# Optimization experiments

Measured on AMD Instinct MI355X. Metric: run time of the kernel, lower is better.

## Reference

```python
import jax, jax.numpy as jnp
import numpy as np

D_MODEL = 1024
N_HEADS = 16
D_FF = 4096
HEAD_DIM = D_MODEL // N_HEADS
LN_EPS = 1e-5


def layer_norm(x, g, b):
    m = jnp.mean(x, axis=-1, keepdims=True)
    v = jnp.mean(jnp.square(x - m), axis=-1, keepdims=True)
    return (x - m) * jax.lax.rsqrt(v + LN_EPS) * g + b


def setup_inputs() -> dict:
    key = jax.random.key(0)
    ks = jax.random.split(key, 16)
    s = 0.02
    d = {
        'x': jax.random.normal(ks[0], (4, 2048, D_MODEL), jnp.float32),
        'Wq': jax.random.normal(ks[1], (D_MODEL, D_MODEL), jnp.float32) * s,
        'bq': jnp.zeros((D_MODEL,), jnp.float32),
        'Wk': jax.random.normal(ks[2], (D_MODEL, D_MODEL), jnp.float32) * s,
        'bk': jnp.zeros((D_MODEL,), jnp.float32),
        'Wv': jax.random.normal(ks[3], (D_MODEL, D_MODEL), jnp.float32) * s,
        'bv': jnp.zeros((D_MODEL,), jnp.float32),
        'Wo': jax.random.normal(ks[4], (D_MODEL, D_MODEL), jnp.float32) * s,
        'bo': jnp.zeros((D_MODEL,), jnp.float32),
        'W1': jax.random.normal(ks[5], (D_FF, D_MODEL), jnp.float32) * s,
        'b1': jnp.zeros((D_FF,), jnp.float32),
        'W2': jax.random.normal(ks[6], (D_MODEL, D_FF), jnp.float32) * s,
        'b2': jnp.zeros((D_MODEL,), jnp.float32),
        'g1': jnp.ones((D_MODEL,), jnp.float32),
        'be1': jnp.zeros((D_MODEL,), jnp.float32),
        'g2': jnp.ones((D_MODEL,), jnp.float32),
        'be2': jnp.zeros((D_MODEL,), jnp.float32),
    }
    return d


def reference(x, Wq, bq, Wk, bk, Wv, bv, Wo, bo, W1, b1, W2, b2, g1, be1, g2, be2):
    B, S, D = x.shape
    H, hd = N_HEADS, HEAD_DIM
    # QKV projections; chunk along d_model -> heads (same as reshape last dim)
    q = (x @ Wq.T + bq).reshape(B, S, H, hd)
    k = (x @ Wk.T + bk).reshape(B, S, H, hd)
    v = (x @ Wv.T + bv).reshape(B, S, H, hd)
    # scaled dot-product attention (no mask, dropout = identity in eval)
    scores = jnp.einsum('bqhd,bkhd->bhqk', q, k) / jnp.sqrt(jnp.float32(hd))
    attn = jax.nn.softmax(scores, axis=-1)
    ctx = jnp.einsum('bhqk,bkhd->bqhd', attn, v).reshape(B, S, D)
    out1 = ctx @ Wo.T + bo
    out = layer_norm(x + out1, g1, be1)
    out2 = jax.nn.relu(out @ W1.T + b1) @ W2.T + b2
    # NOTE: faithful to source bug: second residual uses out1, not out
    return layer_norm(out1 + out2, g2, be2)
```

## Files before the change

kernel.cpp:

```cpp
#include <hip/hip_runtime.h>

typedef __bf16 bf16_t;
typedef __bf16 bf16x8 __attribute__((ext_vector_type(8)));
typedef __bf16 bf16x4 __attribute__((ext_vector_type(4)));
typedef float  f32x4  __attribute__((ext_vector_type(4)));

#define SEQ   2048
#define DMODEL 1024
#define DFF   4096
#define NHEAD 16
#define HDIM  64
#define MTOK  8192

#define QSCALE 0.18033688f
#define THR_LOG2 11.5f

#define MB (size_t)(1024*1024)
static const size_t XB_OFF   = 0;
static const size_t Q_OFF    = 16*MB;
static const size_t K_OFF    = 32*MB;
static const size_t VT_OFF   = 48*MB;
static const size_t FFN1_OFF = 0;
static const size_t CTX_OFF  = 64*MB;
static const size_t OUT1_OFF = 80*MB;
static const size_t LN1_OFF  = 112*MB;
static const size_t WQKV_OFF = 128*MB;
static const size_t WO_OFF   = 134*MB;
static const size_t W1_OFF   = 136*MB;
static const size_t W2_OFF   = 144*MB;

__device__ inline void gload16(const void* g, void* l) {
    __builtin_amdgcn_global_load_lds((__attribute__((address_space(1))) void*)g,
                                     (__attribute__((address_space(3))) void*)l, 16, 0, 0);
}

__global__ __launch_bounds__(256) void cast_bf16_k(const float* __restrict__ s,
                                                   bf16_t* __restrict__ d, int n8) {
    int i = blockIdx.x * 256 + threadIdx.x;
    if (i >= n8) return;
    float4 v0 = ((const float4*)s)[2*i];
    float4 v1 = ((const float4*)s)[2*i+1];
    bf16x8 o;
    o[0]=(bf16_t)v0.x; o[1]=(bf16_t)v0.y; o[2]=(bf16_t)v0.z; o[3]=(bf16_t)v0.w;
    o[4]=(bf16_t)v1.x; o[5]=(bf16_t)v1.y; o[6]=(bf16_t)v1.z; o[7]=(bf16_t)v1.w;
    *(bf16x8*)(d + (size_t)i*8) = o;
}

__global__ __launch_bounds__(256) void concat_bias_k(const float* __restrict__ a,
                                                     const float* __restrict__ b,
                                                     const float* __restrict__ c,
                                                     float* __restrict__ o) {
    int i = blockIdx.x * 256 + threadIdx.x;
    o[i] = (i < 1024) ? a[i] : ((i < 2048) ? b[i - 1024] : c[i - 2048]);
}

template<int EPI>
__global__ __launch_bounds__(256, 2) void gemm_bt(
    const bf16_t* __restrict__ A, const bf16_t* __restrict__ Bm,
    const float* __restrict__ bias, void* __restrict__ out,
    const float* __restrict__ aux, int M, int N, int K, float scale)
{
    __shared__ bf16_t As[128*64];
    __shared__ bf16_t Bs[128*64];
    const int tid = threadIdx.x;
    const int l   = tid & 63;
    const int wid = tid >> 6;
    const int wm  = wid >> 1, wn = wid & 1;
    const int c16 = l & 15,   g  = l >> 4;
    int lin = blockIdx.y * gridDim.x + blockIdx.x;
    int nwg = gridDim.x * gridDim.y;
    int swz = (lin & 7) * (nwg >> 3) + (lin >> 3);
    const long brow = (long)(swz / gridDim.x) * 128;
    const long bcol = (long)(swz % gridDim.x) * 128;

    f32x4 acc[4][4] = {};

    const int nkt = K >> 6;
    for (int kt = 0; kt < nkt; ++kt) {
        __syncthreads();
        const bf16_t* Ag = A  + brow * K + kt*64;
        const bf16_t* Bg = Bm + bcol * K + kt*64;
#pragma unroll
        for (int c = 0; c < 4; ++c) {
            int e   = (c*256 + tid) * 8;
            int row = e >> 6;
            int col = e & 63;
            gload16(Ag + (long)row*K + col, &As[e]);
            gload16(Bg + (long)row*K + col, &Bs[e]);
        }
        __syncthreads();
#pragma unroll
        for (int kk = 0; kk < 2; ++kk) {
            bf16x8 af[4], bfr[4];
#pragma unroll
            for (int mi = 0; mi < 4; ++mi)
                af[mi] = *(const bf16x8*)&As[(wm*64 + mi*16 + c16)*64 + kk*32 + 8*g];
#pragma unroll
            for (int ni = 0; ni < 4; ++ni)
                bfr[ni] = *(const bf16x8*)&Bs[(wn*64 + ni*16 + c16)*64 + kk*32 + 8*g];
#pragma unroll
            for (int mi = 0; mi < 4; ++mi)
#pragma unroll
                for (int ni = 0; ni < 4; ++ni)
                    acc[mi][ni] = __builtin_amdgcn_mfma_f32_16x16x32_bf16(
                        af[mi], bfr[ni], acc[mi][ni], 0, 0, 0);
        }
    }

#pragma unroll
    for (int ni = 0; ni < 4; ++ni) {
        const long c = bcol + wn*64 + ni*16 + c16;
        const float bv = bias[c];
#pragma unroll
        for (int mi = 0; mi < 4; ++mi) {
#pragma unroll
            for (int i = 0; i < 4; ++i) {
                const long r = brow + wm*64 + mi*16 + g*4 + i;
                float v = (acc[mi][ni][i] + bv) * scale;
                if constexpr (EPI == 2) {
                    ((float*)out)[r*N + c] = v;
                } else {
                    ((float*)out)[r*N + c] = v + aux[r*N + c];
                }
            }
        }
    }
}

template<int EPI>
__global__ __launch_bounds__(512, 2) void gemm256(
    const bf16_t* __restrict__ A, const bf16_t* __restrict__ Bm,
    const float* __restrict__ bias, void* __restrict__ out,
    void* __restrict__ out_k, void* __restrict__ out_v,
    int M, int N, int K)
{
    __shared__ alignas(16) char lds[131072];
    const int tid = threadIdx.x;
    const int l   = tid & 63;
    const int wid = tid >> 6;
    const int wm  = wid >> 2, wn = wid & 3;
    const int c16 = l & 15,   g  = l >> 4;
    const int xsw = (c16 & 7) << 4;

    int lin = blockIdx.y * gridDim.x + blockIdx.x;
    int nwg = gridDim.x * gridDim.y;
    int swz = (lin & 7) * (nwg >> 3) + (lin >> 3);
    const long brow = (long)(swz / gridDim.x) * 256;
    const long bcol = (long)(swz % gridDim.x) * 256;

    const int rowloc = tid >> 3;
    const int srcblk = (tid & 7) ^ ((tid >> 3) & 7);
    const bf16_t* Asrc = A  + (brow + rowloc) * (long)K + srcblk * 8;
    const bf16_t* Bsrc = Bm + (bcol + rowloc) * (long)K + srcblk * 8;

    f32x4 acc[8][4] = {};
    const int NKT = K >> 6;

    auto stA = [&](int cur, int t, int j) {
        gload16(Asrc + (long)j*64*K + (long)t*64, lds + cur*65536 + j*8192 + tid*16);
    };
    auto stB = [&](int cur, int t, int j) {
        gload16(Bsrc + (long)j*64*K + (long)t*64, lds + cur*65536 + 32768 + j*8192 + tid*16);
    };

#pragma unroll
    for (int j = 0; j < 4; ++j) stA(0, 0, j);
#pragma unroll
    for (int j = 0; j < 4; ++j) stB(0, 0, j);
#pragma unroll
    for (int j = 0; j < 4; ++j) stA(1, 1, j);
#pragma unroll
    for (int j = 0; j < 4; ++j) stB(1, 1, j);
    asm volatile("s_waitcnt vmcnt(8)" ::: "memory");
    __builtin_amdgcn_sched_barrier(0);
    __builtin_amdgcn_s_barrier();

    int cur = 0;
    for (int t = 0; t < NKT; ++t, cur ^= 1) {
        const char* aL = lds + cur*65536;
        const char* bL = aL + 32768;
        const bool stg = (t + 2 < NKT);
        bf16x8 a0[4][2], a1[4][2], b0[2][2], b1[2][2];

#pragma unroll
        for (int mi = 0; mi < 4; ++mi)
#pragma unroll
            for (int kk = 0; kk < 2; ++kk)
                a0[mi][kk] = *(const bf16x8*)(aL + (wm*128 + mi*16 + c16)*128 + ((kk*64 + 16*g) ^ xsw));
#pragma unroll
        for (int ni = 0; ni < 2; ++ni)
#pragma unroll
            for (int kk = 0; kk < 2; ++kk)
                b0[ni][kk] = *(const bf16x8*)(bL + (wn*64 + ni*16 + c16)*128 + ((kk*64 + 16*g) ^ xsw));
        __builtin_amdgcn_s_barrier();
        asm volatile("s_waitcnt lgkmcnt(0)" ::: "memory");
        __builtin_amdgcn_sched_barrier(0);
        __builtin_amdgcn_s_setprio(1);
#pragma unroll
        for (int mi = 0; mi < 4; ++mi)
#pragma unroll
            for (int ni = 0; ni < 2; ++ni)
#pragma unroll
                for (int kk = 0; kk < 2; ++kk)
                    acc[mi][ni] = __builtin_amdgcn_mfma_f32_16x16x32_bf16(a0[mi][kk], b0[ni][kk], acc[mi][ni], 0, 0, 0);
        __builtin_amdgcn_s_setprio(0);
        __builtin_amdgcn_s_barrier();

#pragma unroll
        for (int ni = 0; ni < 2; ++ni)
#pragma unroll
            for (int kk = 0; kk < 2; ++kk)
                b1[ni][kk] = *(const bf16x8*)(bL + (wn*64 + (ni+2)*16 + c16)*128 + ((kk*64 + 16*g) ^ xsw));
        if (stg) { stA(cur, t+2, 0); stA(cur, t+2, 2); }
        __builtin_amdgcn_s_barrier();
        asm volatile("s_waitcnt lgkmcnt(0)" ::: "memory");
        __builtin_amdgcn_sched_barrier(0);
        __builtin_amdgcn_s_setprio(1);
#pragma unroll
        for (int mi = 0; mi < 4; ++mi)
#pragma unroll
            for (int ni = 0; ni < 2; ++ni)
#pragma unroll
                for (int kk = 0; kk < 2; ++kk)
                    acc[mi][ni+2] = __builtin_amdgcn_mfma_f32_16x16x32_bf16(a0[mi][kk], b1[ni][kk], acc[mi][ni+2], 0, 0, 0);
        __builtin_amdgcn_s_setprio(0);
        __builtin_amdgcn_s_barrier();

#pragma unroll
        for (int mi = 0; mi < 4; ++mi)
#pragma unroll
            for (int kk = 0; kk < 2; ++kk)
                a1[mi][kk] = *(const bf16x8*)(aL + (wm*128 + (mi+4)*16 + c16)*128 + ((kk*64 + 16*g) ^ xsw));
        if (stg) { stB(cur, t+2, 0); stB(cur, t+2, 1); }
        __builtin_amdgcn_s_barrier();
        asm volatile("s_waitcnt lgkmcnt(0)" ::: "memory");
        __builtin_amdgcn_sched_barrier(0);
        __builtin_amdgcn_s_setprio(1);
#pragma unroll
        for (int mi = 0; mi < 4; ++mi)
#pragma unroll
            for (int ni = 0; ni < 2; ++ni)
#pragma unroll
                for (int kk = 0; kk < 2; ++kk)
                    acc[mi+4][ni] = __builtin_amdgcn_mfma_f32_16x16x32_bf16(a1[mi][kk], b0[ni][kk], acc[mi+4][ni], 0, 0, 0);
        __builtin_amdgcn_s_setprio(0);
        __builtin_amdgcn_s_barrier();

        if (stg) { stA(cur, t+2, 1); stA(cur, t+2, 3); stB(cur, t+2, 2); stB(cur, t+2, 3); }
        __builtin_amdgcn_s_barrier();
        __builtin_amdgcn_s_setprio(1);
#pragma unroll
        for (int mi = 0; mi < 4; ++mi)
#pragma unroll
            for (int ni = 0; ni < 2; ++ni)
#pragma unroll
                for (int kk = 0; kk < 2; ++kk)
                    acc[mi+4][ni+2] = __builtin_amdgcn_mfma_f32_16x16x32_bf16(a1[mi][kk], b1[ni][kk], acc[mi+4][ni+2], 0, 0, 0);
        __builtin_amdgcn_s_setprio(0);
        if (stg)                asm volatile("s_waitcnt vmcnt(8)" ::: "memory");
        else if (t < NKT - 1)   asm volatile("s_waitcnt vmcnt(0)" ::: "memory");
        __builtin_amdgcn_sched_barrier(0);
        __builtin_amdgcn_s_barrier();
    }

#pragma unroll
    for (int ni = 0; ni < 4; ++ni) {
        const long c = bcol + wn*64 + ni*16 + c16;
        const float bv = bias[c];
#pragma unroll
        for (int mi = 0; mi < 8; ++mi) {
#pragma unroll
            for (int i = 0; i < 4; ++i) {
                const long r = brow + wm*128 + mi*16 + g*4 + i;
                float v = acc[mi][ni][i] + bv;
                if constexpr (EPI == 3) {
                    ((bf16_t*)out)[r*N + c] = (bf16_t)fmaxf(v, 0.f);
                } else {
                    const int mat = (int)(c >> 10);
                    const int hc  = (int)(c & 1023);
                    const long bb = r >> 11, sidx = r & (SEQ-1);
                    const long hb = bb*NHEAD + (hc >> 6);
                    if (mat == 0)
                        ((bf16_t*)out)[(hb*SEQ + sidx)*HDIM + (hc & 63)] = (bf16_t)(v * QSCALE);
                    else if (mat == 1)
                        ((bf16_t*)out_k)[(hb*SEQ + sidx)*HDIM + (hc & 63)] = (bf16_t)v;
                    else
                        ((bf16_t*)out_v)[(hb*HDIM + (hc & 63))*SEQ + sidx] = (bf16_t)v;
                }
            }
        }
    }
}

__device__ __forceinline__ void kload(bf16x8 (&dst)[4][2], const bf16_t* kb0,
                                      int ktt, int c16, int g) {
    const bf16_t* kbase = kb0 + (size_t)ktt*64*HDIM;
#pragma unroll
    for (int jk = 0; jk < 4; ++jk)
#pragma unroll
        for (int ks = 0; ks < 2; ++ks)
            dst[jk][ks] = *(const bf16x8*)(kbase + (size_t)(16*jk + c16)*HDIM + ks*32 + 8*g);
}

__device__ __forceinline__ void vload(bf16x8 (&vr)[4][2], const bf16_t* vt0,
                                      int ktt, int c16, int g) {
#pragma unroll
    for (int nf = 0; nf < 4; ++nf)
#pragma unroll
        for (int ks = 0; ks < 2; ++ks)
            vr[nf][ks] = *(const bf16x8*)(vt0 + (size_t)(16*nf + c16)*SEQ + ktt*64 + ks*32 + 8*g);
}

__device__ __forceinline__ void qk1(f32x4 (&s)[4], const bf16x8 (&kr)[4][2],
                                    const bf16x8 (&aqf)[2]) {
    const f32x4 z = {0.f, 0.f, 0.f, 0.f};
    __builtin_amdgcn_s_setprio(1);
#pragma unroll
    for (int jk = 0; jk < 4; ++jk) {
        s[jk] = __builtin_amdgcn_mfma_f32_16x16x32_bf16(kr[jk][0], aqf[0], z, 0, 0, 0);
        s[jk] = __builtin_amdgcn_mfma_f32_16x16x32_bf16(kr[jk][1], aqf[1], s[jk], 0, 0, 0);
    }
    __builtin_amdgcn_s_setprio(0);
}

__device__ __forceinline__ void sm1(f32x4 (&s)[4], f32x4 (&accf)[4],
                                    float& m, float& ls, int g) {
    f32x4 t01, t23, t03;
#pragma unroll
    for (int i = 0; i < 4; ++i) {
        t01[i] = fmaxf(s[0][i], s[1][i]);
        t23[i] = fmaxf(s[2][i], s[3][i]);
    }
#pragma unroll
    for (int i = 0; i < 4; ++i) t03[i] = fmaxf(t01[i], t23[i]);
    float lmax = fmaxf(fmaxf(t03[0], t03[1]), fmaxf(t03[2], t03[3]));
    if (__any(lmax > m + THR_LOG2)) {
        float pm = lmax;
        pm = fmaxf(pm, __shfl_xor(pm, 16, 64));
        pm = fmaxf(pm, __shfl_xor(pm, 32, 64));
        float mn   = fmaxf(m, pm);
        float corr = __builtin_exp2f(m - mn);
        ls *= corr;
        m   = mn;
        float c0 = __shfl(corr, 4*g + 0, 64);
        float c1 = __shfl(corr, 4*g + 1, 64);
        float c2 = __shfl(corr, 4*g + 2, 64);
        float c3 = __shfl(corr, 4*g + 3, 64);
#pragma unroll
        for (int nf = 0; nf < 4; ++nf) {
            accf[nf][0] *= c0; accf[nf][1] *= c1;
            accf[nf][2] *= c2; accf[nf][3] *= c3;
        }
    }
#pragma unroll
    for (int jk = 0; jk < 4; ++jk)
#pragma unroll
        for (int i = 0; i < 4; ++i)
            s[jk][i] = __builtin_exp2f(s[jk][i] - m);
    f32x4 r01, r23, r;
#pragma unroll
    for (int i = 0; i < 4; ++i) {
        r01[i] = s[0][i] + s[1][i];
        r23[i] = s[2][i] + s[3][i];
    }
#pragma unroll
    for (int i = 0; i < 4; ++i) r[i] = r01[i] + r23[i];
    ls += (r[0] + r[1]) + (r[2] + r[3]);
}

__device__ __forceinline__ void pw1(const f32x4 (&s)[4], char* buf, int qf, int c16, int g) {
#pragma unroll
    for (int jk = 0; jk < 4; ++jk) {
        bf16x4 pk;
        pk[0]=(bf16_t)s[jk][0]; pk[1]=(bf16_t)s[jk][1];
        pk[2]=(bf16_t)s[jk][2]; pk[3]=(bf16_t)s[jk][3];
        *(bf16x4*)(buf + (qf*16 + c16)*128 + ((32*jk + 8*g) ^ ((c16 & 7) << 4))) = pk;
    }
}

__device__ __forceinline__ void pv1(f32x4 (&accf)[4], const bf16x8 (&vr)[4][2],
                                    const char* buf, int qf, int c16, int g) {
    __builtin_amdgcn_s_setprio(1);
#pragma unroll
    for (int ks = 0; ks < 2; ++ks) {
        bf16x8 pa = *(const bf16x8*)(buf + (qf*16 + c16)*128 + ((ks*64 + 16*g) ^ ((c16 & 7) << 4)));
#pragma unroll
        for (int nf = 0; nf < 4; ++nf)
            accf[nf] = __builtin_amdgcn_mfma_f32_16x16x32_bf16(pa, vr[nf][ks], accf[nf], 0, 0, 0);
    }
    __builtin_amdgcn_s_setprio(0);
}

__global__ __launch_bounds__(256, 2) void attn_k(
    const bf16_t* __restrict__ qb, const bf16_t* __restrict__ kb,
    const bf16_t* __restrict__ vt, bf16_t* __restrict__ ctx)
{
    const int id  = blockIdx.x;
    const int idx = id >> 3;
    const int bh  = (id & 7) + 8 * (idx & 7);
    const int qt  = idx >> 3;
    const int w   = threadIdx.x >> 6;
    const int l   = threadIdx.x & 63;
    const int c16 = l & 15, g = l >> 4;
    const int q0  = qt*256 + w*64;

    __shared__ char Ps[4*16384];
    char* myP = &Ps[w*16384];

    bf16x8 aq[4][2];
#pragma unroll
    for (int qf = 0; qf < 4; ++qf) {
        const bf16_t* qrow = qb + ((size_t)bh*SEQ + q0 + qf*16 + c16)*HDIM;
        aq[qf][0] = *(const bf16x8*)(qrow + 8*g);
        aq[qf][1] = *(const bf16x8*)(qrow + 32 + 8*g);
    }

    const bf16_t* kb0 = kb + (size_t)bh*SEQ*HDIM;
    const bf16_t* vt0 = vt + (size_t)bh*HDIM*SEQ;

    f32x4 acc[4][4] = {};
    float m[4]  = {-1e30f, -1e30f, -1e30f, -1e30f};
    float ls[4] = {0.f, 0.f, 0.f, 0.f};

    bf16x8 kr[4][2], vr[4][2];
    f32x4 s[4];

    kload(kr, kb0, 0, c16, g);

    const int NT = SEQ/64;
    for (int t = 0; t < NT; ++t) {
        char* buf = myP + (t & 1) * 8192;
        qk1(s, kr, aq[0]); sm1(s, acc[0], m[0], ls[0], g); pw1(s, buf, 0, c16, g);
        qk1(s, kr, aq[1]); sm1(s, acc[1], m[1], ls[1], g); pw1(s, buf, 1, c16, g);
        qk1(s, kr, aq[2]); sm1(s, acc[2], m[2], ls[2], g); pw1(s, buf, 2, c16, g);
        qk1(s, kr, aq[3]);
        if (t + 1 < NT) kload(kr, kb0, t + 1, c16, g);
        vload(vr, vt0, t, c16, g);
        __builtin_amdgcn_sched_barrier(0);
        sm1(s, acc[3], m[3], ls[3], g); pw1(s, buf, 3, c16, g);
        asm volatile("s_waitcnt lgkmcnt(0)" ::: "memory");
        __builtin_amdgcn_sched_barrier(0);
        pv1(acc[0], vr, buf, 0, c16, g);
        pv1(acc[1], vr, buf, 1, c16, g);
        pv1(acc[2], vr, buf, 2, c16, g);
        pv1(acc[3], vr, buf, 3, c16, g);
        asm volatile("" ::: "memory");
    }

    const int b = bh >> 4, h = bh & 15;
#pragma unroll
    for (int qf = 0; qf < 4; ++qf) {
        float lst = ls[qf];
        lst += __shfl_xor(lst, 16, 64);
        lst += __shfl_xor(lst, 32, 64);
        float i0 = 1.0f / __shfl(lst, 4*g + 0, 64);
        float i1 = 1.0f / __shfl(lst, 4*g + 1, 64);
        float i2 = 1.0f / __shfl(lst, 4*g + 2, 64);
        float i3 = 1.0f / __shfl(lst, 4*g + 3, 64);
#pragma unroll
        for (int nf = 0; nf < 4; ++nf) {
            long col = (size_t)h*HDIM + nf*16 + c16;
            long rb  = (size_t)b*SEQ + q0 + qf*16 + 4*g;
            ctx[(rb + 0)*DMODEL + col] = (bf16_t)(acc[qf][nf][0] * i0);
            ctx[(rb + 1)*DMODEL + col] = (bf16_t)(acc[qf][nf][1] * i1);
            ctx[(rb + 2)*DMODEL + col] = (bf16_t)(acc[qf][nf][2] * i2);
            ctx[(rb + 3)*DMODEL + col] = (bf16_t)(acc[qf][nf][3] * i3);
        }
    }
}

__global__ __launch_bounds__(256) void ln_k(
    const float* __restrict__ a, const float* __restrict__ b,
    const float* __restrict__ g, const float* __restrict__ be,
    float* __restrict__ of, bf16_t* __restrict__ ob)
{
    const long row = blockIdx.x;
    const int tid = threadIdx.x;
    float4 v = ((const float4*)(a + row*DMODEL))[tid];
    if (b) {
        float4 u = ((const float4*)(b + row*DMODEL))[tid];
        v.x += u.x; v.y += u.y; v.z += u.z; v.w += u.w;
    }
    float s = v.x + v.y + v.z + v.w;
    float q = v.x*v.x + v.y*v.y + v.z*v.z + v.w*v.w;
#pragma unroll
    for (int msk = 1; msk < 64; msk <<= 1) {
        s += __shfl_xor(s, msk, 64);
        q += __shfl_xor(q, msk, 64);
    }
    __shared__ float sb[4], qb2[4];
    int w = tid >> 6, lid = tid & 63;
    if (lid == 0) { sb[w] = s; qb2[w] = q; }
    __syncthreads();
    s = sb[0] + sb[1] + sb[2] + sb[3];
    q = qb2[0] + qb2[1] + qb2[2] + qb2[3];
    float mean = s * (1.f/1024.f);
    float var  = q * (1.f/1024.f) - mean*mean;
    float rs   = rsqrtf(var + 1e-5f);
    float4 gv = ((const float4*)g)[tid];
    float4 bv = ((const float4*)be)[tid];
    float o0 = (v.x-mean)*rs*gv.x + bv.x;
    float o1 = (v.y-mean)*rs*gv.y + bv.y;
    float o2 = (v.z-mean)*rs*gv.z + bv.z;
    float o3 = (v.w-mean)*rs*gv.w + bv.w;
    if (ob) {
        bf16x4 o; o[0]=(bf16_t)o0; o[1]=(bf16_t)o1; o[2]=(bf16_t)o2; o[3]=(bf16_t)o3;
        *(bf16x4*)(ob + row*DMODEL + tid*4) = o;
    } else {
        float4 o = make_float4(o0, o1, o2, o3);
        ((float4*)(of + row*DMODEL))[tid] = o;
    }
}

extern "C" void kernel_launch(void* const* d_in, const int* in_sizes, int n_in,
                              void* d_out, int out_size, void* d_ws, size_t ws_size,
                              hipStream_t stream)
{
    const float* x   = (const float*)d_in[0];
    const float* Wq  = (const float*)d_in[1];
    const float* bq  = (const float*)d_in[2];
    const float* Wk  = (const float*)d_in[3];
    const float* bk  = (const float*)d_in[4];
    const float* Wv  = (const float*)d_in[5];
    const float* bvv = (const float*)d_in[6];
    const float* Wo  = (const float*)d_in[7];
    const float* bo  = (const float*)d_in[8];
    const float* W1  = (const float*)d_in[9];
    const float* b1  = (const float*)d_in[10];
    const float* W2  = (const float*)d_in[11];
    const float* b2  = (const float*)d_in[12];
    const float* g1  = (const float*)d_in[13];
    const float* be1 = (const float*)d_in[14];
    const float* g2  = (const float*)d_in[15];
    const float* be2 = (const float*)d_in[16];

    char* ws = (char*)d_ws;
    bf16_t* xb   = (bf16_t*)(ws + XB_OFF);
    bf16_t* qbuf = (bf16_t*)(ws + Q_OFF);
    bf16_t* kbuf = (bf16_t*)(ws + K_OFF);
    bf16_t* vtb  = (bf16_t*)(ws + VT_OFF);
    bf16_t* ffn1 = (bf16_t*)(ws + FFN1_OFF);
    bf16_t* ctxb = (bf16_t*)(ws + CTX_OFF);
    float*  out1 = (float*)(ws + OUT1_OFF);
    bf16_t* ln1b = (bf16_t*)(ws + LN1_OFF);
    bf16_t* wqkv = (bf16_t*)(ws + WQKV_OFF);
    bf16_t* wob  = (bf16_t*)(ws + WO_OFF);
    bf16_t* w1b  = (bf16_t*)(ws + W1_OFF);
    bf16_t* w2b  = (bf16_t*)(ws + W2_OFF);
    float*  biasc= (float*)(ws + OUT1_OFF);
    float*  dout = (float*)d_out;

    auto cast = [&](const float* s, bf16_t* d, long n) {
        int n8 = (int)(n / 8);
        cast_bf16_k<<<(n8 + 255)/256, 256, 0, stream>>>(s, d, n8);
    };
    cast(x,  xb,  (long)MTOK*DMODEL);
    cast(Wq, wqkv,                        (long)DMODEL*DMODEL);
    cast(Wk, wqkv + (long)DMODEL*DMODEL,  (long)DMODEL*DMODEL);
    cast(Wv, wqkv + 2L*DMODEL*DMODEL,     (long)DMODEL*DMODEL);
    cast(Wo, wob, (long)DMODEL*DMODEL);
    cast(W1, w1b, (long)DFF*DMODEL);
    cast(W2, w2b, (long)DMODEL*DFF);
    concat_bias_k<<<12, 256, 0, stream>>>(bq, bk, bvv, biasc);

    gemm256<5><<<dim3(3*DMODEL/256, MTOK/256), dim3(512), 0, stream>>>(
        xb, wqkv, biasc, qbuf, kbuf, vtb, MTOK, 3*DMODEL, DMODEL);
    attn_k<<<dim3(512), dim3(256), 0, stream>>>(qbuf, kbuf, vtb, ctxb);
    gemm_bt<2><<<dim3(DMODEL/128, MTOK/128), dim3(256), 0, stream>>>(
        ctxb, wob, bo, out1, nullptr, MTOK, DMODEL, DMODEL, 1.f);
    ln_k<<<MTOK, dim3(256), 0, stream>>>(x, out1, g1, be1, nullptr, ln1b);
    gemm256<3><<<dim3(DFF/256, MTOK/256), dim3(512), 0, stream>>>(
        ln1b, w1b, b1, ffn1, nullptr, nullptr, MTOK, DFF, DMODEL);
    gemm_bt<4><<<dim3(DMODEL/128, MTOK/128), dim3(256), 0, stream>>>(
        ffn1, w2b, b2, out1, out1, MTOK, DMODEL, DFF, 1.f);
    ln_k<<<MTOK, dim3(256), 0, stream>>>(out1, nullptr, g2, be2, dout, nullptr);
}
```

Baseline: 576.0 us.

## Share K/V tiles via LDS in attention and merge weight casts into one kernel

The attention kernel now stages each 64-row K and V^T tile into double-buffered shared memory with async global-to-LDS loads. All four waves read those tiles from LDS instead of each wave loading them from global memory. Each wave now handles 32 queries instead of 64, so the grid doubles to 1024 blocks and occupancy is raised to 3 blocks per SM, at the cost of a block-wide barrier every tile. Separately, the seven fp32-to-bf16 cast launches are folded into a single kernel that picks the source by index range, removing launch overhead.

New measurement: 485.6 us. 15.7% less time.

```diff
diff --git a/kernel.cpp b/kernel.cpp
--- a/kernel.cpp
+++ b/kernel.cpp
@@ -34,16 +34,29 @@
                                      (__attribute__((address_space(3))) void*)l, 16, 0, 0);
 }
 
-__global__ __launch_bounds__(256) void cast_bf16_k(const float* __restrict__ s,
-                                                   bf16_t* __restrict__ d, int n8) {
-    int i = blockIdx.x * 256 + threadIdx.x;
-    if (i >= n8) return;
-    float4 v0 = ((const float4*)s)[2*i];
-    float4 v1 = ((const float4*)s)[2*i+1];
+__global__ __launch_bounds__(256) void cast_all_k(
+    const float* __restrict__ x,  const float* __restrict__ Wq,
+    const float* __restrict__ Wk, const float* __restrict__ Wv,
+    const float* __restrict__ Wo, const float* __restrict__ W1,
+    const float* __restrict__ W2,
+    bf16_t* __restrict__ xb, bf16_t* __restrict__ wqkv,
+    bf16_t* __restrict__ wob, bf16_t* __restrict__ w1b, bf16_t* __restrict__ w2b)
+{
+    long i = (long)blockIdx.x * 256 + threadIdx.x;
+    const float* src; bf16_t* dst; long j;
+    if      (i < 1048576) { src = x;  dst = xb;             j = i; }
+    else if (i < 1179648) { src = Wq; dst = wqkv;           j = i - 1048576; }
+    else if (i < 1310720) { src = Wk; dst = wqkv + 1048576; j = i - 1179648; }
+    else if (i < 1441792) { src = Wv; dst = wqkv + 2097152; j = i - 1310720; }
+    else if (i < 1572864) { src = Wo; dst = wob;            j = i - 1441792; }
+    else if (i < 2097152) { src = W1; dst = w1b;            j = i - 1572864; }
+    else                  { src = W2; dst = w2b;            j = i - 2097152; }
+    float4 v0 = ((const float4*)src)[2*j];
+    float4 v1 = ((const float4*)src)[2*j+1];
     bf16x8 o;
     o[0]=(bf16_t)v0.x; o[1]=(bf16_t)v0.y; o[2]=(bf16_t)v0.z; o[3]=(bf16_t)v0.w;
     o[4]=(bf16_t)v1.x; o[5]=(bf16_t)v1.y; o[6]=(bf16_t)v1.z; o[7]=(bf16_t)v1.w;
-    *(bf16x8*)(d + (size_t)i*8) = o;
+    *(bf16x8*)(dst + j*8) = o;
 }
 
 __global__ __launch_bounds__(256) void concat_bias_k(const float* __restrict__ a,
@@ -292,25 +305,6 @@
     }
 }
 
-__device__ __forceinline__ void kload(bf16x8 (&dst)[4][2], const bf16_t* kb0,
-                                      int ktt, int c16, int g) {
-    const bf16_t* kbase = kb0 + (size_t)ktt*64*HDIM;
-#pragma unroll
-    for (int jk = 0; jk < 4; ++jk)
-#pragma unroll
-        for (int ks = 0; ks < 2; ++ks)
-            dst[jk][ks] = *(const bf16x8*)(kbase + (size_t)(16*jk + c16)*HDIM + ks*32 + 8*g);
-}
-
-__device__ __forceinline__ void vload(bf16x8 (&vr)[4][2], const bf16_t* vt0,
-                                      int ktt, int c16, int g) {
-#pragma unroll
-    for (int nf = 0; nf < 4; ++nf)
-#pragma unroll
-        for (int ks = 0; ks < 2; ++ks)
-            vr[nf][ks] = *(const bf16x8*)(vt0 + (size_t)(16*nf + c16)*SEQ + ktt*64 + ks*32 + 8*g);
-}
-
 __device__ __forceinline__ void qk1(f32x4 (&s)[4], const bf16x8 (&kr)[4][2],
                                     const bf16x8 (&aqf)[2]) {
     const f32x4 z = {0.f, 0.f, 0.f, 0.f};
@@ -391,7 +385,7 @@
     __builtin_amdgcn_s_setprio(0);
 }
 
-__global__ __launch_bounds__(256, 2) void attn_k(
+__global__ __launch_bounds__(256, 3) void attn_k(
     const bf16_t* __restrict__ qb, const bf16_t* __restrict__ kb,
     const bf16_t* __restrict__ vt, bf16_t* __restrict__ ctx)
 {
@@ -399,17 +393,20 @@
     const int idx = id >> 3;
     const int bh  = (id & 7) + 8 * (idx & 7);
     const int qt  = idx >> 3;
-    const int w   = threadIdx.x >> 6;
-    const int l   = threadIdx.x & 63;
+    const int tid = threadIdx.x;
+    const int w   = tid >> 6;
+    const int l   = tid & 63;
     const int c16 = l & 15, g = l >> 4;
-    const int q0  = qt*256 + w*64;
-
-    __shared__ char Ps[4*16384];
-    char* myP = &Ps[w*16384];
-
-    bf16x8 aq[4][2];
-#pragma unroll
-    for (int qf = 0; qf < 4; ++qf) {
+    const int q0  = qt*128 + w*32;
+    const int xsw = (c16 & 7) << 4;
+
+    __shared__ alignas(16) char kvLds[2][16384];
+    __shared__ alignas(16) char Ps[4][4096];
+    char* myP = Ps[w];
+
+    bf16x8 aq[2][2];
+#pragma unroll
+    for (int qf = 0; qf < 2; ++qf) {
         const bf16_t* qrow = qb + ((size_t)bh*SEQ + q0 + qf*16 + c16)*HDIM;
         aq[qf][0] = *(const bf16x8*)(qrow + 8*g);
         aq[qf][1] = *(const bf16x8*)(qrow + 32 + 8*g);
@@ -418,38 +415,60 @@
     const bf16_t* kb0 = kb + (size_t)bh*SEQ*HDIM;
     const bf16_t* vt0 = vt + (size_t)bh*HDIM*SEQ;
 
-    f32x4 acc[4][4] = {};
-    float m[4]  = {-1e30f, -1e30f, -1e30f, -1e30f};
-    float ls[4] = {0.f, 0.f, 0.f, 0.f};
-
-    bf16x8 kr[4][2], vr[4][2];
+    const int r0 = tid >> 3;
+    const int r1 = (256 + tid) >> 3;
+    const int b0 = (tid & 7) ^ (r0 & 7);
+    const int b1 = (tid & 7) ^ (r1 & 7);
+    const bf16_t* ksrc0 = kb0 + (size_t)r0*HDIM + b0*8;
+    const bf16_t* ksrc1 = kb0 + (size_t)r1*HDIM + b1*8;
+    const bf16_t* vsrc0 = vt0 + (size_t)r0*SEQ + b0*8;
+    const bf16_t* vsrc1 = vt0 + (size_t)r1*SEQ + b1*8;
+
+    auto stage = [&](int buf, int t) {
+        char* kd = kvLds[buf];
+        char* vd = kd + 8192;
+        gload16(ksrc0 + (size_t)t*64*HDIM, kd + tid*16);
+        gload16(ksrc1 + (size_t)t*64*HDIM, kd + 4096 + tid*16);
+        gload16(vsrc0 + t*64, vd + tid*16);
+        gload16(vsrc1 + t*64, vd + 4096 + tid*16);
+    };
+
+    f32x4 acc[2][4] = {};
+    float m[2]  = {-1e30f, -1e30f};
+    float ls[2] = {0.f, 0.f};
     f32x4 s[4];
 
-    kload(kr, kb0, 0, c16, g);
+    stage(0, 0);
+    __syncthreads();
 
     const int NT = SEQ/64;
     for (int t = 0; t < NT; ++t) {
-        char* buf = myP + (t & 1) * 8192;
-        qk1(s, kr, aq[0]); sm1(s, acc[0], m[0], ls[0], g); pw1(s, buf, 0, c16, g);
-        qk1(s, kr, aq[1]); sm1(s, acc[1], m[1], ls[1], g); pw1(s, buf, 1, c16, g);
-        qk1(s, kr, aq[2]); sm1(s, acc[2], m[2], ls[2], g); pw1(s, buf, 2, c16, g);
-        qk1(s, kr, aq[3]);
-        if (t + 1 < NT) kload(kr, kb0, t + 1, c16, g);
-        vload(vr, vt0, t, c16, g);
-        __builtin_amdgcn_sched_barrier(0);
-        sm1(s, acc[3], m[3], ls[3], g); pw1(s, buf, 3, c16, g);
+        const char* kd = kvLds[t & 1];
+        const char* vd = kd + 8192;
+        if (t + 1 < NT) stage((t + 1) & 1, t + 1);
+        bf16x8 kr[4][2], vr[4][2];
+#pragma unroll
+        for (int jk = 0; jk < 4; ++jk)
+#pragma unroll
+            for (int ks = 0; ks < 2; ++ks)
+                kr[jk][ks] = *(const bf16x8*)(kd + (16*jk + c16)*128 + ((ks*64 + 16*g) ^ xsw));
+#pragma unroll
+        for (int nf = 0; nf < 4; ++nf)
+#pragma unroll
+            for (int ks = 0; ks < 2; ++ks)
+                vr[nf][ks] = *(const bf16x8*)(vd + (16*nf + c16)*128 + ((ks*64 + 16*g) ^ xsw));
+        qk1(s, kr, aq[0]); sm1(s, acc[0], m[0], ls[0], g); pw1(s, myP, 0, c16, g);
+        qk1(s, kr, aq[1]); sm1(s, acc[1], m[1], ls[1], g); pw1(s, myP, 1, c16, g);
         asm volatile("s_waitcnt lgkmcnt(0)" ::: "memory");
         __builtin_amdgcn_sched_barrier(0);
-        pv1(acc[0], vr, buf, 0, c16, g);
-        pv1(acc[1], vr, buf, 1, c16, g);
-        pv1(acc[2], vr, buf, 2, c16, g);
-        pv1(acc[3], vr, buf, 3, c16, g);
-        asm volatile("" ::: "memory");
+        pv1(acc[0], vr, myP, 0, c16, g);
+        pv1(acc[1], vr, myP, 1, c16, g);
+        __syncthreads();
     }
 
     const int b = bh >> 4, h = bh & 15;
 #pragma unroll
-    for (int qf = 0; qf < 4; ++qf) {
+    for (int qf = 0; qf < 2; ++qf) {
         float lst = ls[qf];
         lst += __shfl_xor(lst, 16, 64);
         lst += __shfl_xor(lst, 32, 64);
@@ -550,22 +569,13 @@
     float*  biasc= (float*)(ws + OUT1_OFF);
     float*  dout = (float*)d_out;
 
-    auto cast = [&](const float* s, bf16_t* d, long n) {
-        int n8 = (int)(n / 8);
-        cast_bf16_k<<<(n8 + 255)/256, 256, 0, stream>>>(s, d, n8);
-    };
-    cast(x,  xb,  (long)MTOK*DMODEL);
-    cast(Wq, wqkv,                        (long)DMODEL*DMODEL);
-    cast(Wk, wqkv + (long)DMODEL*DMODEL,  (long)DMODEL*DMODEL);
-    cast(Wv, wqkv + 2L*DMODEL*DMODEL,     (long)DMODEL*DMODEL);
-    cast(Wo, wob, (long)DMODEL*DMODEL);
-    cast(W1, w1b, (long)DFF*DMODEL);
-    cast(W2, w2b, (long)DMODEL*DFF);
+    cast_all_k<<<10240, 256, 0, stream>>>(x, Wq, Wk, Wv, Wo, W1, W2,
+                                          xb, wqkv, wob, w1b, w2b);
     concat_bias_k<<<12, 256, 0, stream>>>(bq, bk, bvv, biasc);
 
     gemm256<5><<<dim3(3*DMODEL/256, MTOK/256), dim3(512), 0, stream>>>(
         xb, wqkv, biasc, qbuf, kbuf, vtb, MTOK, 3*DMODEL, DMODEL);
-    attn_k<<<dim3(512), dim3(256), 0, stream>>>(qbuf, kbuf, vtb, ctxb);
+    attn_k<<<dim3(1024), dim3(256), 0, stream>>>(qbuf, kbuf, vtb, ctxb);
     gemm_bt<2><<<dim3(DMODEL/128, MTOK/128), dim3(256), 0, stream>>>(
         ctxb, wob, bo, out1, nullptr, MTOK, DMODEL, DMODEL, 1.f);
     ln_k<<<MTOK, dim3(256), 0, stream>>>(x, out1, g1, be1, nullptr, ln1b);
```
